# Optimization experiments

Measured on AMD Instinct MI355X. Metric: run time of the kernel, lower is better.

The kernel has to match this reference:

```python
import jax, jax.numpy as jnp
import numpy as np

B, S, D = 2, 2048, 1024
H = 16
HEAD_DIM = 64          # matches head_dim init arg; D // H == 64
HALF_WINDOW = 32       # local_window_size // 2
SCALE = HEAD_DIM ** -0.5


def setup_inputs() -> dict:
    key = jax.random.key(0)
    ks = jax.random.split(key, 6)
    std = 1.0 / np.sqrt(D)
    return {
        "x": jax.random.normal(ks[0], (B, S, D), dtype=jnp.float32),
        "Wq": jax.random.normal(ks[1], (D, D), dtype=jnp.float32) * std,
        "Wk": jax.random.normal(ks[2], (D, D), dtype=jnp.float32) * std,
        "Wv": jax.random.normal(ks[3], (D, D), dtype=jnp.float32) * std,
        "Wo": jax.random.normal(ks[4], (D, D), dtype=jnp.float32) * std,
        "bo": jnp.zeros((D,), dtype=jnp.float32),
    }


def reference(x, Wq, Wk, Wv, Wo, bo):
    b, s, d = x.shape
    h, hd = H, d // H

    def split_heads(y):  # [b, s, d] -> [b, h, s, hd]
        return y.reshape(b, s, h, hd).transpose(0, 2, 1, 3)

    q = split_heads(x @ Wq) * SCALE
    k = split_heads(x @ Wk)
    v = split_heads(x @ Wv)

    # dense scores [b, h, s, s] (module materializes full O(S^2) matrix)
    scores = jnp.einsum("bhqd,bhkd->bhqk", q, k)

    # local window |i-j| <= HALF_WINDOW combined with causal j <= i
    i = jnp.arange(s)
    local = jnp.abs(i[:, None] - i[None, :]) <= HALF_WINDOW
    causal = i[None, :] <= i[:, None]
    mask = local & causal  # [s, s]
    scores = jnp.where(mask[None, None, :, :], scores, -jnp.inf)

    attn = jax.nn.softmax(scores, axis=-1)  # diagonal always valid -> no NaN
    out = jnp.einsum("bhqk,bhkd->bhqd", attn, v)
    out = out.transpose(0, 2, 1, 3).reshape(b, s, d)  # merge heads
    return out @ Wo + bo
```

## Files before the change

kernel.cpp:

```cpp
#include <hip/hip_runtime.h>
#include <hip/hip_bf16.h>

typedef __bf16 bf16_t;
typedef __bf16 bf16x8 __attribute__((ext_vector_type(8)));
typedef __bf16 bf16x4 __attribute__((ext_vector_type(4)));
typedef float  f32x4  __attribute__((ext_vector_type(4)));

#define B_   2
#define S_   2048
#define D_   1024
#define H_   16
#define HD_  64
#define HW   32
#define SCALE_ 0.125f

__device__ __forceinline__ void gl_lds16(const bf16_t* g, bf16_t* l) {
  __builtin_amdgcn_global_load_lds(
      (const __attribute__((address_space(1))) void*)g,
      (__attribute__((address_space(3))) void*)l, 16, 0, 0);
}

__global__ __launch_bounds__(256) void k_conv(const float* __restrict__ X,
                                              const float* __restrict__ W0,
                                              const float* __restrict__ W1,
                                              const float* __restrict__ W2,
                                              const float* __restrict__ W3,
                                              bf16_t* __restrict__ Xb,
                                              bf16_t* __restrict__ Wt) {
  __shared__ bf16_t t[64][72];
  int bid = blockIdx.x;
  int tid = threadIdx.x;
  if (bid < 2048) {
    int i = bid * 256 + tid;
    const float4 a = ((const float4*)X)[i * 2];
    const float4 b = ((const float4*)X)[i * 2 + 1];
    bf16x8 r;
    r[0] = (bf16_t)a.x; r[1] = (bf16_t)a.y; r[2] = (bf16_t)a.z; r[3] = (bf16_t)a.w;
    r[4] = (bf16_t)b.x; r[5] = (bf16_t)b.y; r[6] = (bf16_t)b.z; r[7] = (bf16_t)b.w;
    ((bf16x8*)Xb)[i] = r;
    return;
  }
  int wb = bid - 2048;
  int wsel = wb >> 8;
  const float* W = (wsel == 0) ? W0 : (wsel == 1) ? W1 : (wsel == 2) ? W2 : W3;
  bf16_t* dst = Wt + (size_t)wsel * D_ * D_;
  int tile = wb & 255;
  int k0 = (tile >> 4) * 64, n0 = (tile & 15) * 64;
  int r = tid >> 4, c4 = (tid & 15) * 4;
#pragma unroll
  for (int i = 0; i < 4; ++i) {
    int row = i * 16 + r;
    float4 v = *(const float4*)(W + (size_t)(k0 + row) * D_ + n0 + c4);
    t[row][c4 + 0] = (bf16_t)v.x;
    t[row][c4 + 1] = (bf16_t)v.y;
    t[row][c4 + 2] = (bf16_t)v.z;
    t[row][c4 + 3] = (bf16_t)v.w;
  }
  __syncthreads();
#pragma unroll
  for (int i = 0; i < 4; ++i) {
    int row = i * 16 + r;
    bf16x4 o;
    o[0] = t[c4 + 0][row];
    o[1] = t[c4 + 1][row];
    o[2] = t[c4 + 2][row];
    o[3] = t[c4 + 3][row];
    *(bf16x4*)(dst + (size_t)(n0 + row) * D_ + k0 + c4) = o;
  }
}

__global__ __launch_bounds__(256) void k_gemm_qkv(const bf16_t* __restrict__ X,
                                                  const bf16_t* __restrict__ Wt,
                                                  bf16_t* __restrict__ Q,
                                                  bf16_t* __restrict__ Kb,
                                                  bf16_t* __restrict__ V) {
  __shared__ bf16_t sA[3 * 128 * 32];
  __shared__ bf16_t sB[3 * 128 * 32];
  int bid = blockIdx.x;
  int mt = bid & 31, nt = bid >> 5;
  int wsel = nt >> 3;
  int n0 = (nt & 7) * 128, m0 = mt * 128;
  const bf16_t* Wp = Wt + (size_t)wsel * D_ * D_;
  int tid = threadIdx.x, lane = tid & 63, wave = tid >> 6;
  int wr = (wave >> 1) * 64, wc = (wave & 1) * 64;
  int r0 = wave * 32 + (lane >> 2);
  int ce = (((lane & 3) ^ ((lane >> 3) & 3))) * 8;
  const bf16_t* gA0 = X + (size_t)(m0 + r0) * D_ + ce;
  const bf16_t* gB0 = Wp + (size_t)(n0 + r0) * D_ + ce;
  int lofs = wave * 1024;
#define QSTAGE_(bi, kt) do { \
    gl_lds16(gA0 + (kt), sA + (bi) * 4096 + lofs);        \
    gl_lds16(gA0 + (kt) + (size_t)16 * D_, sA + (bi) * 4096 + lofs + 512); \
    gl_lds16(gB0 + (kt), sB + (bi) * 4096 + lofs);        \
    gl_lds16(gB0 + (kt) + (size_t)16 * D_, sB + (bi) * 4096 + lofs + 512); \
  } while (0)
  f32x4 acc[4][4] = {};
  int rl = lane & 15, hi = lane >> 4;
  int cofs = (hi ^ ((rl >> 1) & 3)) * 8;
  QSTAGE_(0, 0);
  QSTAGE_(1, 32);
  asm volatile("s_waitcnt vmcnt(4)" ::: "memory");
  __builtin_amdgcn_sched_barrier(0);
  __builtin_amdgcn_s_barrier();
  asm volatile("" ::: "memory");
  int cur = 0;
  for (int t = 0; t < 32; ++t) {
    const bf16_t* pA = sA + cur * 4096;
    const bf16_t* pB = sB + cur * 4096;
    bf16x8 af[4], bfr[4];
#pragma unroll
    for (int m = 0; m < 4; ++m)
      af[m] = *(const bf16x8*)&pA[(wr + m * 16 + rl) * 32 + cofs];
#pragma unroll
    for (int n = 0; n < 4; ++n)
      bfr[n] = *(const bf16x8*)&pB[(wc + n * 16 + rl) * 32 + cofs];
    int sb = cur + 2; if (sb >= 3) sb -= 3;
    if (t + 2 < 32) QSTAGE_(sb, (t + 2) * 32);
    __builtin_amdgcn_s_setprio(1);
#pragma unroll
    for (int m = 0; m < 4; ++m)
#pragma unroll
      for (int n = 0; n < 4; ++n)
        acc[m][n] = __builtin_amdgcn_mfma_f32_16x16x32_bf16(af[m], bfr[n], acc[m][n], 0, 0, 0);
    __builtin_amdgcn_s_setprio(0);
    if (t < 30) {
      asm volatile("s_waitcnt vmcnt(4)" ::: "memory");
    } else if (t == 30) {
      asm volatile("s_waitcnt vmcnt(0)" ::: "memory");
    }
    if (t < 31) {
      __builtin_amdgcn_sched_barrier(0);
      __builtin_amdgcn_s_barrier();
      asm volatile("" ::: "memory");
    }
    if (++cur == 3) cur = 0;
  }
#undef QSTAGE_
  float qscale = (wsel == 0) ? SCALE_ : 1.0f;
#pragma unroll
  for (int m = 0; m < 4; ++m) {
#pragma unroll
    for (int n = 0; n < 4; ++n) {
#pragma unroll
      for (int r = 0; r < 4; ++r) {
        int gm = m0 + wr + m * 16 + (lane >> 4) * 4 + r;
        int gn = n0 + wc + n * 16 + rl;
        int b = gm >> 11, s = gm & 2047;
        int h = gn >> 6, hd = gn & 63;
        bf16_t val = (bf16_t)(acc[m][n][r] * qscale);
        if (wsel == 0)
          Q[(((size_t)(b * H_ + h)) * S_ + s) * HD_ + hd] = val;
        else if (wsel == 1)
          Kb[(((size_t)(b * H_ + h)) * S_ + s) * HD_ + hd] = val;
        else
          V[(((size_t)(b * H_ + h)) * HD_ + hd) * S_ + s] = val;
      }
    }
  }
}

__global__ __launch_bounds__(256) void k_gemm_out(const bf16_t* __restrict__ A,
                                                  const bf16_t* __restrict__ Wp,
                                                  const float* __restrict__ bo,
                                                  float* __restrict__ out) {
  __shared__ bf16_t sA[64 * 32];
  __shared__ bf16_t sB[128 * 32];
  int bid = blockIdx.x;
  int mt = bid & 63, nt = bid >> 6;
  int n0 = nt * 128, m0 = mt * 64;
  int tid = threadIdx.x, lane = tid & 63, wave = tid >> 6;
  int wc = wave * 32;
  int crow = lane >> 2, ccol = (lane & 3) * 8;
  const bf16_t* gsrc0; bf16_t* ldst0;
  const bf16_t* gsrc1; bf16_t* ldst1;
  const bf16_t* gsrc2; bf16_t* ldst2;
#pragma unroll
  for (int j = 0; j < 3; ++j) {
    int c = wave * 3 + j;
    const bf16_t* g; bf16_t* l;
    if (c < 4) {
      g = A + (size_t)(m0 + c * 16 + crow) * D_ + ccol;
      l = sA + c * 512;
    } else {
      g = Wp + (size_t)(n0 + (c - 4) * 16 + crow) * D_ + ccol;
      l = sB + (c - 4) * 512;
    }
    if (j == 0) { gsrc0 = g; ldst0 = l; }
    else if (j == 1) { gsrc1 = g; ldst1 = l; }
    else { gsrc2 = g; ldst2 = l; }
  }
  f32x4 acc[4][2] = {};
  int kq = (lane >> 4) * 8, rl = lane & 15, hi = lane >> 4;
  for (int kt = 0; kt < D_; kt += 32) {
    __syncthreads();
    gl_lds16(gsrc0 + kt, ldst0);
    gl_lds16(gsrc1 + kt, ldst1);
    gl_lds16(gsrc2 + kt, ldst2);
    __syncthreads();
    bf16x8 af[4], bfr[2];
#pragma unroll
    for (int m = 0; m < 4; ++m)
      af[m] = *(const bf16x8*)&sA[(m * 16 + rl) * 32 + kq];
#pragma unroll
    for (int n = 0; n < 2; ++n)
      bfr[n] = *(const bf16x8*)&sB[(wc + n * 16 + rl) * 32 + kq];
#pragma unroll
    for (int m = 0; m < 4; ++m)
#pragma unroll
      for (int n = 0; n < 2; ++n)
        acc[m][n] = __builtin_amdgcn_mfma_f32_16x16x32_bf16(af[m], bfr[n], acc[m][n], 0, 0, 0);
  }
#pragma unroll
  for (int m = 0; m < 4; ++m) {
#pragma unroll
    for (int n = 0; n < 2; ++n) {
#pragma unroll
      for (int r = 0; r < 4; ++r) {
        int gm = m0 + m * 16 + hi * 4 + r;
        int gn = n0 + wc + n * 16 + rl;
        out[(size_t)gm * D_ + gn] = acc[m][n][r] + bo[gn];
      }
    }
  }
}

#define QB 64
#define KW 112
#define KLP 68
#define VTP 116

__global__ __launch_bounds__(256) void k_attn(const bf16_t* __restrict__ Q,
                                              const bf16_t* __restrict__ K,
                                              const bf16_t* __restrict__ Vt,
                                              bf16_t* __restrict__ O) {
  __shared__ bf16_t sK[KW][KLP];
  __shared__ bf16_t sV[HD_][VTP];
  __shared__ bf16_t sP[4][16][KLP];
  int bid = blockIdx.x;
  int qb = bid & 31, bh = bid >> 5;
  int q0 = qb * QB;
  const bf16_t* Kp = K + (size_t)bh * S_ * HD_;
  const bf16_t* Vp = Vt + (size_t)bh * HD_ * S_;
  const bf16_t* Qp = Q + (size_t)bh * S_ * HD_;
  int tid = threadIdx.x;
  int lane = tid & 63, wave = tid >> 6;
  int rl = lane & 15, hi = lane >> 4;
  int wk0b = q0 - HW;
  bf16x8 qf0 = *(const bf16x8*)(Qp + (size_t)(q0 + wave * 16 + rl) * HD_ + hi * 8);
  bf16x8 qf1 = *(const bf16x8*)(Qp + (size_t)(q0 + wave * 16 + rl) * HD_ + 32 + hi * 8);
  for (int idx = tid; idx < KW * 8; idx += 256) {
    int row = idx >> 3, c8 = (idx & 7) * 8;
    int kg = wk0b + row;
    kg = kg < 0 ? 0 : (kg > S_ - 1 ? S_ - 1 : kg);
    *(bf16x8*)&sK[row][c8] = *(const bf16x8*)(Kp + (size_t)kg * HD_ + c8);
  }
  for (int idx = tid; idx < HD_ * 14; idx += 256) {
    int row = idx / 14, c8 = (idx % 14) * 8;
    int ks = wk0b + c8;
    ks = ks < 0 ? 0 : (ks > S_ - 8 ? S_ - 8 : ks);
    *(bf16x8*)&sV[row][c8] = *(const bf16x8*)(Vp + (size_t)row * S_ + ks);
  }
  __syncthreads();
  int wko = wave * 16;
  f32x4 accs[4] = {};
#pragma unroll
  for (int kb = 0; kb < 4; ++kb) {
    bf16x8 kf = *(const bf16x8*)&sK[wko + kb * 16 + rl][hi * 8];
    accs[kb] = __builtin_amdgcn_mfma_f32_16x16x32_bf16(kf, qf0, accs[kb], 0, 0, 0);
  }
#pragma unroll
  for (int kb = 0; kb < 4; ++kb) {
    bf16x8 kf = *(const bf16x8*)&sK[wko + kb * 16 + rl][32 + hi * 8];
    accs[kb] = __builtin_amdgcn_mfma_f32_16x16x32_bf16(kf, qf1, accs[kb], 0, 0, 0);
  }
  float p[4][4];
  float mx = -1e30f;
#pragma unroll
  for (int kb = 0; kb < 4; ++kb) {
#pragma unroll
    for (int r = 0; r < 4; ++r) {
      int kl = kb * 16 + hi * 4 + r;
      bool valid = (kl >= rl) && (kl <= rl + HW) && (wk0b + wko + kl >= 0);
      float s = valid ? accs[kb][r] : -1e30f;
      p[kb][r] = s;
      mx = fmaxf(mx, s);
    }
  }
  mx = fmaxf(mx, __shfl_xor(mx, 16));
  mx = fmaxf(mx, __shfl_xor(mx, 32));
  float sum = 0.f;
#pragma unroll
  for (int kb = 0; kb < 4; ++kb)
#pragma unroll
    for (int r = 0; r < 4; ++r) {
      p[kb][r] = __expf(p[kb][r] - mx);
      sum += p[kb][r];
    }
  sum += __shfl_xor(sum, 16);
  sum += __shfl_xor(sum, 32);
  float inv = 1.f / sum;
#pragma unroll
  for (int kb = 0; kb < 4; ++kb) {
    bf16x4 pv;
#pragma unroll
    for (int r = 0; r < 4; ++r) pv[r] = (bf16_t)(p[kb][r] * inv);
    *(bf16x4*)&sP[wave][rl][kb * 16 + hi * 4] = pv;
  }
  f32x4 acco[4] = {};
#pragma unroll
  for (int ks = 0; ks < 2; ++ks) {
    bf16x8 aP = *(const bf16x8*)&sP[wave][rl][ks * 32 + hi * 8];
#pragma unroll
    for (int n = 0; n < 4; ++n) {
      bf16x8 bV = *(const bf16x8*)&sV[n * 16 + rl][wko + ks * 32 + hi * 8];
      acco[n] = __builtin_amdgcn_mfma_f32_16x16x32_bf16(aP, bV, acco[n], 0, 0, 0);
    }
  }
  int b = bh >> 4, h = bh & 15;
#pragma unroll
  for (int n = 0; n < 4; ++n) {
#pragma unroll
    for (int r = 0; r < 4; ++r) {
      int qgl = q0 + wave * 16 + hi * 4 + r;
      int d = n * 16 + rl;
      O[((size_t)(b * S_ + qgl)) * D_ + h * HD_ + d] = (bf16_t)acco[n][r];
    }
  }
}

extern "C" void kernel_launch(void* const* d_in, const int* in_sizes, int n_in,
                              void* d_out, int out_size, void* d_ws, size_t ws_size,
                              hipStream_t stream) {
  const float* x  = (const float*)d_in[0];
  const float* Wq = (const float*)d_in[1];
  const float* Wk = (const float*)d_in[2];
  const float* Wv = (const float*)d_in[3];
  const float* Wo = (const float*)d_in[4];
  const float* bo = (const float*)d_in[5];
  float* out = (float*)d_out;
  char* ws = (char*)d_ws;
  bf16_t* xb = (bf16_t*)(ws);
  bf16_t* wt = (bf16_t*)(ws + (size_t)(8 << 20));
  bf16_t* qb = (bf16_t*)(ws + (size_t)(16 << 20));
  bf16_t* kb = (bf16_t*)(ws + (size_t)(24 << 20));
  bf16_t* vb = (bf16_t*)(ws + (size_t)(32 << 20));
  bf16_t* ob = (bf16_t*)(ws + (size_t)(40 << 20));

  hipLaunchKernelGGL(k_conv, dim3(3072), dim3(256), 0, stream,
                     x, Wq, Wk, Wv, Wo, xb, wt);
  hipLaunchKernelGGL(k_gemm_qkv, dim3(768), dim3(256), 0, stream, xb, wt, qb, kb, vb);
  hipLaunchKernelGGL(k_attn, dim3(1024), dim3(256), 0, stream, qb, kb, vb, ob);
  hipLaunchKernelGGL(k_gemm_out, dim3(512), dim3(256), 0, stream,
                     ob, wt + (size_t)3 * D_ * D_, bo, out);
}
```

Baseline: 81.65 us.

## Coalesce V transpose stores via LDS and double attention query tile

The QKV GEMM epilogue now stages the V tile through shared memory so the transposed V layout is written with 16-byte vector stores instead of scattered 2-byte stores. The attention kernel now processes 128 queries per block in two passes over a larger K/V window, which halves the grid and cuts redundant halo loads. It also trims the score MFMAs from four key blocks to three and zero-pads the unused P columns. The cost is more shared memory per block, extra barriers in the epilogue, and fewer blocks to spread across CUs.

```diff
diff --git a/kernel.cpp b/kernel.cpp
--- a/kernel.cpp
+++ b/kernel.cpp
@@ -136,24 +136,48 @@
     if (++cur == 3) cur = 0;
   }
 #undef QSTAGE_
-  float qscale = (wsel == 0) ? SCALE_ : 1.0f;
-#pragma unroll
-  for (int m = 0; m < 4; ++m) {
-#pragma unroll
-    for (int n = 0; n < 4; ++n) {
-#pragma unroll
-      for (int r = 0; r < 4; ++r) {
-        int gm = m0 + wr + m * 16 + (lane >> 4) * 4 + r;
-        int gn = n0 + wc + n * 16 + rl;
-        int b = gm >> 11, s = gm & 2047;
+  if (wsel < 2) {
+    float qscale = (wsel == 0) ? SCALE_ : 1.0f;
+    bf16_t* Dst = wsel ? Kb : Q;
+#pragma unroll
+    for (int m = 0; m < 4; ++m) {
+#pragma unroll
+      for (int n = 0; n < 4; ++n) {
+#pragma unroll
+        for (int r = 0; r < 4; ++r) {
+          int gm = m0 + wr + m * 16 + hi * 4 + r;
+          int gn = n0 + wc + n * 16 + rl;
+          int b = gm >> 11, s = gm & 2047;
+          int h = gn >> 6, hd = gn & 63;
+          Dst[(((size_t)(b * H_ + h)) * S_ + s) * HD_ + hd] = (bf16_t)(acc[m][n][r] * qscale);
+        }
+      }
+    }
+  } else {
+    bf16_t* bounce = sA;
+#pragma unroll
+    for (int hh = 0; hh < 2; ++hh) {
+      __syncthreads();
+      if ((wave & 1) == hh) {
+#pragma unroll
+        for (int m = 0; m < 4; ++m)
+#pragma unroll
+          for (int n = 0; n < 4; ++n)
+#pragma unroll
+            for (int r = 0; r < 4; ++r)
+              bounce[(n * 16 + rl) * 136 + wr + m * 16 + hi * 4 + r] = (bf16_t)acc[m][n][r];
+      }
+      __syncthreads();
+#pragma unroll
+      for (int ps = 0; ps < 4; ++ps) {
+        int idx = ps * 256 + tid;
+        int row = idx >> 4, c8 = (idx & 15) * 8;
+        bf16x8 v = *(const bf16x8*)&bounce[row * 136 + c8];
+        int gn = n0 + hh * 64 + row;
         int h = gn >> 6, hd = gn & 63;
-        bf16_t val = (bf16_t)(acc[m][n][r] * qscale);
-        if (wsel == 0)
-          Q[(((size_t)(b * H_ + h)) * S_ + s) * HD_ + hd] = val;
-        else if (wsel == 1)
-          Kb[(((size_t)(b * H_ + h)) * S_ + s) * HD_ + hd] = val;
-        else
-          V[(((size_t)(b * H_ + h)) * HD_ + hd) * S_ + s] = val;
+        int gmS = m0 + c8;
+        int b2 = gmS >> 11, s0 = gmS & 2047;
+        *(bf16x8*)&V[(((size_t)(b2 * H_ + h)) * HD_ + hd) * S_ + s0] = v;
       }
     }
   }
@@ -224,10 +248,11 @@
   }
 }
 
-#define QB 64
-#define KW 112
+#define QB 128
+#define KW 160
+#define VW 176
 #define KLP 68
-#define VTP 116
+#define VTP 180
 
 __global__ __launch_bounds__(256) void k_attn(const bf16_t* __restrict__ Q,
                                               const bf16_t* __restrict__ K,
@@ -237,7 +262,7 @@
   __shared__ bf16_t sV[HD_][VTP];
   __shared__ bf16_t sP[4][16][KLP];
   int bid = blockIdx.x;
-  int qb = bid & 31, bh = bid >> 5;
+  int qb = bid & 15, bh = bid >> 4;
   int q0 = qb * QB;
   const bf16_t* Kp = K + (size_t)bh * S_ * HD_;
   const bf16_t* Vp = Vt + (size_t)bh * HD_ * S_;
@@ -246,84 +271,93 @@
   int lane = tid & 63, wave = tid >> 6;
   int rl = lane & 15, hi = lane >> 4;
   int wk0b = q0 - HW;
-  bf16x8 qf0 = *(const bf16x8*)(Qp + (size_t)(q0 + wave * 16 + rl) * HD_ + hi * 8);
-  bf16x8 qf1 = *(const bf16x8*)(Qp + (size_t)(q0 + wave * 16 + rl) * HD_ + 32 + hi * 8);
   for (int idx = tid; idx < KW * 8; idx += 256) {
     int row = idx >> 3, c8 = (idx & 7) * 8;
     int kg = wk0b + row;
     kg = kg < 0 ? 0 : (kg > S_ - 1 ? S_ - 1 : kg);
     *(bf16x8*)&sK[row][c8] = *(const bf16x8*)(Kp + (size_t)kg * HD_ + c8);
   }
-  for (int idx = tid; idx < HD_ * 14; idx += 256) {
-    int row = idx / 14, c8 = (idx % 14) * 8;
+  for (int idx = tid; idx < HD_ * (VW / 8); idx += 256) {
+    int row = idx / (VW / 8), c8 = (idx % (VW / 8)) * 8;
     int ks = wk0b + c8;
     ks = ks < 0 ? 0 : (ks > S_ - 8 ? S_ - 8 : ks);
     *(bf16x8*)&sV[row][c8] = *(const bf16x8*)(Vp + (size_t)row * S_ + ks);
   }
   __syncthreads();
-  int wko = wave * 16;
-  f32x4 accs[4] = {};
-#pragma unroll
-  for (int kb = 0; kb < 4; ++kb) {
-    bf16x8 kf = *(const bf16x8*)&sK[wko + kb * 16 + rl][hi * 8];
-    accs[kb] = __builtin_amdgcn_mfma_f32_16x16x32_bf16(kf, qf0, accs[kb], 0, 0, 0);
-  }
-#pragma unroll
-  for (int kb = 0; kb < 4; ++kb) {
-    bf16x8 kf = *(const bf16x8*)&sK[wko + kb * 16 + rl][32 + hi * 8];
-    accs[kb] = __builtin_amdgcn_mfma_f32_16x16x32_bf16(kf, qf1, accs[kb], 0, 0, 0);
-  }
-  float p[4][4];
-  float mx = -1e30f;
-#pragma unroll
-  for (int kb = 0; kb < 4; ++kb) {
-#pragma unroll
-    for (int r = 0; r < 4; ++r) {
-      int kl = kb * 16 + hi * 4 + r;
-      bool valid = (kl >= rl) && (kl <= rl + HW) && (wk0b + wko + kl >= 0);
-      float s = valid ? accs[kb][r] : -1e30f;
-      p[kb][r] = s;
-      mx = fmaxf(mx, s);
-    }
-  }
-  mx = fmaxf(mx, __shfl_xor(mx, 16));
-  mx = fmaxf(mx, __shfl_xor(mx, 32));
-  float sum = 0.f;
-#pragma unroll
-  for (int kb = 0; kb < 4; ++kb)
-#pragma unroll
-    for (int r = 0; r < 4; ++r) {
-      p[kb][r] = __expf(p[kb][r] - mx);
-      sum += p[kb][r];
-    }
-  sum += __shfl_xor(sum, 16);
-  sum += __shfl_xor(sum, 32);
-  float inv = 1.f / sum;
-#pragma unroll
-  for (int kb = 0; kb < 4; ++kb) {
-    bf16x4 pv;
-#pragma unroll
-    for (int r = 0; r < 4; ++r) pv[r] = (bf16_t)(p[kb][r] * inv);
-    *(bf16x4*)&sP[wave][rl][kb * 16 + hi * 4] = pv;
-  }
-  f32x4 acco[4] = {};
-#pragma unroll
-  for (int ks = 0; ks < 2; ++ks) {
-    bf16x8 aP = *(const bf16x8*)&sP[wave][rl][ks * 32 + hi * 8];
+  int b = bh >> 4, h = bh & 15;
+#pragma unroll
+  for (int qi = 0; qi < 2; ++qi) {
+    int wko = qi * 64 + wave * 16;
+    bf16x8 qf0 = *(const bf16x8*)(Qp + (size_t)(q0 + wko + rl) * HD_ + hi * 8);
+    bf16x8 qf1 = *(const bf16x8*)(Qp + (size_t)(q0 + wko + rl) * HD_ + 32 + hi * 8);
+    f32x4 accs[3] = {};
+#pragma unroll
+    for (int kb = 0; kb < 3; ++kb) {
+      bf16x8 kf = *(const bf16x8*)&sK[wko + kb * 16 + rl][hi * 8];
+      accs[kb] = __builtin_amdgcn_mfma_f32_16x16x32_bf16(kf, qf0, accs[kb], 0, 0, 0);
+    }
+#pragma unroll
+    for (int kb = 0; kb < 3; ++kb) {
+      bf16x8 kf = *(const bf16x8*)&sK[wko + kb * 16 + rl][32 + hi * 8];
+      accs[kb] = __builtin_amdgcn_mfma_f32_16x16x32_bf16(kf, qf1, accs[kb], 0, 0, 0);
+    }
+    float p[3][4];
+    float mx = -1e30f;
+#pragma unroll
+    for (int kb = 0; kb < 3; ++kb) {
+#pragma unroll
+      for (int r = 0; r < 4; ++r) {
+        int kl = kb * 16 + hi * 4 + r;
+        bool valid = (kl >= rl) && (kl <= rl + HW) && (wk0b + wko + kl >= 0);
+        float s = valid ? accs[kb][r] : -1e30f;
+        p[kb][r] = s;
+        mx = fmaxf(mx, s);
+      }
+    }
+    mx = fmaxf(mx, __shfl_xor(mx, 16));
+    mx = fmaxf(mx, __shfl_xor(mx, 32));
+    float sum = 0.f;
+#pragma unroll
+    for (int kb = 0; kb < 3; ++kb)
+#pragma unroll
+      for (int r = 0; r < 4; ++r) {
+        p[kb][r] = __expf(p[kb][r] - mx);
+        sum += p[kb][r];
+      }
+    sum += __shfl_xor(sum, 16);
+    sum += __shfl_xor(sum, 32);
+    float inv = 1.f / sum;
+#pragma unroll
+    for (int kb = 0; kb < 3; ++kb) {
+      bf16x4 pv;
+#pragma unroll
+      for (int r = 0; r < 4; ++r) pv[r] = (bf16_t)(p[kb][r] * inv);
+      *(bf16x4*)&sP[wave][rl][kb * 16 + hi * 4] = pv;
+    }
+    {
+      bf16x4 z4;
+#pragma unroll
+      for (int r = 0; r < 4; ++r) z4[r] = (bf16_t)0.f;
+      *(bf16x4*)&sP[wave][rl][48 + hi * 4] = z4;
+    }
+    f32x4 acco[4] = {};
+#pragma unroll
+    for (int ks = 0; ks < 2; ++ks) {
+      bf16x8 aP = *(const bf16x8*)&sP[wave][rl][ks * 32 + hi * 8];
+#pragma unroll
+      for (int n = 0; n < 4; ++n) {
+        bf16x8 bV = *(const bf16x8*)&sV[n * 16 + rl][wko + ks * 32 + hi * 8];
+        acco[n] = __builtin_amdgcn_mfma_f32_16x16x32_bf16(aP, bV, acco[n], 0, 0, 0);
+      }
+    }
 #pragma unroll
     for (int n = 0; n < 4; ++n) {
-      bf16x8 bV = *(const bf16x8*)&sV[n * 16 + rl][wko + ks * 32 + hi * 8];
-      acco[n] = __builtin_amdgcn_mfma_f32_16x16x32_bf16(aP, bV, acco[n], 0, 0, 0);
-    }
-  }
-  int b = bh >> 4, h = bh & 15;
-#pragma unroll
-  for (int n = 0; n < 4; ++n) {
-#pragma unroll
-    for (int r = 0; r < 4; ++r) {
-      int qgl = q0 + wave * 16 + hi * 4 + r;
-      int d = n * 16 + rl;
-      O[((size_t)(b * S_ + qgl)) * D_ + h * HD_ + d] = (bf16_t)acco[n][r];
+#pragma unroll
+      for (int r = 0; r < 4; ++r) {
+        int qgl = q0 + wko + hi * 4 + r;
+        int d = n * 16 + rl;
+        O[((size_t)(b * S_ + qgl)) * D_ + h * HD_ + d] = (bf16_t)acco[n][r];
+      }
     }
   }
 }
@@ -349,7 +383,7 @@
   hipLaunchKernelGGL(k_conv, dim3(3072), dim3(256), 0, stream,
                      x, Wq, Wk, Wv, Wo, xb, wt);
   hipLaunchKernelGGL(k_gemm_qkv, dim3(768), dim3(256), 0, stream, xb, wt, qb, kb, vb);
-  hipLaunchKernelGGL(k_attn, dim3(1024), dim3(256), 0, stream, qb, kb, vb, ob);
+  hipLaunchKernelGGL(k_attn, dim3(512), dim3(256), 0, stream, qb, kb, vb, ob);
   hipLaunchKernelGGL(k_gemm_out, dim3(512), dim3(256), 0, stream,
                      ob, wt + (size_t)3 * D_ * D_, bo, out);
 }
```

New measurement: 79.72 us, median of 2. 2.4% less time.
